# Kernel tuning notes

Hardware: AMD Instinct MI355X
Metric: run time of the kernel (lower is better)

The kernel has to match this reference:

```python
import jax, jax.numpy as jnp
import numpy as np

B_, S_, D_ = 2, 1024, 768
EXPAND, HEADDIM, DSTATE = 2, 64, 64
DINNER = EXPAND * D_            # 1536
NHEADS = DINNER // HEADDIM      # 24
DMLP = int(2.5 * D_)            # 1920
PROJ = 2 * DINNER + 2 * NHEADS * DSTATE + NHEADS + NHEADS * (DSTATE // 2)  # 6936


def rms_norm(x, w, eps=1e-5):
    return x * jax.lax.rsqrt(jnp.mean(x * x, axis=-1, keepdims=True) + eps) * w


def apply_rope(x, angles):
    # x: (..., d_state), angles: (..., d_state//2)
    x1 = x[..., 0::2]
    x2 = x[..., 1::2]
    c, s = jnp.cos(angles), jnp.sin(angles)
    even = c * x1 - s * x2
    odd = s * x1 + c * x2
    return jnp.stack([even, odd], axis=-1).reshape(x.shape)


def ssm_scan(x, A, Bm, Cm):
    # x: (b,s,h,p), A: (b,s,h), Bm/Cm: (b,s,h,n)
    b, s, h, p = x.shape
    n = Bm.shape[-1]

    def step(hstate, inp):
        x_t, A_t, B_t, C_t = inp
        hstate = hstate * jnp.exp(A_t)[:, :, None, None] + jnp.einsum('bhn,bhp->bhpn', B_t, x_t)
        y_t = jnp.einsum('bhpn,bhn->bhp', hstate, C_t)
        return hstate, y_t

    h0 = jnp.zeros((b, h, p, n), dtype=x.dtype)
    xs = (jnp.swapaxes(x, 0, 1), jnp.swapaxes(A, 0, 1),
          jnp.swapaxes(Bm, 0, 1), jnp.swapaxes(Cm, 0, 1))
    _, ys = jax.lax.scan(step, h0, xs)
    return jnp.swapaxes(ys, 0, 1)  # (b,s,h,p)


def setup_inputs() -> dict:
    key = jax.random.key(0)
    ks = jax.random.split(key, 16)
    sc = 0.02
    return {
        'x': jax.random.normal(ks[0], (B_, S_, D_), dtype=jnp.float32),
        'norm1_w': jnp.ones((D_,), jnp.float32),
        'norm2_w': jnp.ones((D_,), jnp.float32),
        'in_proj_w': jax.random.normal(ks[1], (PROJ, D_), jnp.float32) * sc,
        'out_proj_w': jax.random.normal(ks[2], (D_, DINNER), jnp.float32) * sc,
        'A_log': jax.random.uniform(ks[3], (NHEADS,), jnp.float32, -4.0, -1.0),
        'D': jnp.ones((NHEADS,), jnp.float32),
        'dt_bias': jax.random.uniform(ks[4], (NHEADS,), jnp.float32, 0.001, 0.1),
        'B_bias': jnp.ones((1, NHEADS, DSTATE), jnp.float32),
        'C_bias': jnp.ones((1, NHEADS, DSTATE), jnp.float32),
        'Bnorm_w': jnp.ones((DSTATE,), jnp.float32),
        'Cnorm_w': jnp.ones((DSTATE,), jnp.float32),
        'mlp_gate_w': jax.random.normal(ks[5], (DMLP, D_), jnp.float32) * sc,
        'mlp_up_w': jax.random.normal(ks[6], (DMLP, D_), jnp.float32) * sc,
        'mlp_down_w': jax.random.normal(ks[7], (D_, DMLP), jnp.float32) * sc,
    }


def reference(x, norm1_w, norm2_w, in_proj_w, out_proj_w, A_log, D, dt_bias,
              B_bias, C_bias, Bnorm_w, Cnorm_w, mlp_gate_w, mlp_up_w, mlp_down_w):
    b, s, _ = x.shape
    h = rms_norm(x, norm1_w)
    proj = jnp.einsum('bsd,od->bso', h, in_proj_w)
    i = 0
    z = proj[..., i:i + DINNER]; i += DINNER
    x_ssm = proj[..., i:i + DINNER]; i += DINNER
    Bm = proj[..., i:i + NHEADS * DSTATE].reshape(b, s, NHEADS, DSTATE); i += NHEADS * DSTATE
    Cm = proj[..., i:i + NHEADS * DSTATE].reshape(b, s, NHEADS, DSTATE); i += NHEADS * DSTATE
    dt = proj[..., i:i + NHEADS]; i += NHEADS
    theta = proj[..., i:].reshape(b, s, NHEADS, DSTATE // 2)

    dt = jax.nn.softplus(dt + dt_bias)                 # (b,s,h)
    A = -jnp.exp(A_log) * dt                           # (b,s,h)
    alpha = jnp.exp(A)
    gamma = (alpha - 1.0) / (A + 1e-6) * 0.5 + 1.0

    Bm = rms_norm(Bm, Bnorm_w) + B_bias
    Cm = rms_norm(Cm, Cnorm_w) + C_bias
    cum_theta = jnp.cumsum(dt[..., None] * theta, axis=1)
    Bm = apply_rope(Bm, cum_theta)
    Cm = apply_rope(Cm, cum_theta)

    x_ssm = x_ssm.reshape(b, s, NHEADS, HEADDIM)
    x_scaled = x_ssm * gamma[..., None]
    y = ssm_scan(x_scaled, A, Bm, Cm)                  # (b,s,h,p)
    skip = (D[None, None, :] * x_ssm.sum(-1))[..., None]  # (b,s,h,1)
    y = (y + skip).reshape(b, s, DINNER)
    y = y * (z * jax.nn.sigmoid(z))
    y = jnp.einsum('bsi,oi->bso', y, out_proj_w)
    x = x + y
    h2 = rms_norm(x, norm2_w)
    g = jnp.einsum('bsd,od->bso', h2, mlp_gate_w)
    u = jnp.einsum('bsd,od->bso', h2, mlp_up_w)
    mlp = jnp.einsum('bsi,oi->bso', (g * jax.nn.sigmoid(g)) * u, mlp_down_w)
    return x + mlp
```

## Files before the change

kernel.cpp:

```cpp
#include <hip/hip_runtime.h>

typedef unsigned short u16;
typedef __attribute__((ext_vector_type(8))) short short8;
typedef __attribute__((ext_vector_type(4))) float f32x4;

constexpr int B_N    = 2;
constexpr int SEQ    = 1024;
constexpr int DMODEL = 768;
constexpr int DINNER = 1536;
constexpr int NH     = 24;
constexpr int DMLP   = 1920;
constexpr int NPROJ  = 6936;
constexpr int PP     = 7040;
constexpr int MROWS  = B_N * SEQ;
constexpr int NCHUNK = 16;
constexpr int CLEN   = 64;

__device__ __forceinline__ u16 f2bf(float f) {
  union { float f; unsigned u; } x; x.f = f;
  unsigned r = x.u + 0x7fffu + ((x.u >> 16) & 1u);
  return (u16)(r >> 16);
}
__device__ __forceinline__ float bf2f(u16 b) {
  union { unsigned u; float f; } x; x.u = ((unsigned)b) << 16; return x.f;
}

__device__ __forceinline__ void gld_lds16(const u16* g, u16* l) {
  __builtin_amdgcn_global_load_lds((const __attribute__((address_space(1))) void*)g,
                                   (__attribute__((address_space(3))) void*)l, 16, 0, 0);
}

__device__ __forceinline__ short8 frag(const u16* base, int row, int cb) {
  return *(const short8*)(base + row * 64 + ((cb ^ (row & 7)) << 3));
}
__device__ __forceinline__ int swz_idx(int row, int e) {
  return (((e >> 3) ^ (row & 7)) << 3) | (e & 7);
}

constexpr size_t E0  = (size_t)PP * DMODEL;
constexpr size_t E0s = (size_t)NPROJ * DMODEL;
constexpr size_t E1  = (size_t)DMODEL * DINNER;
constexpr size_t E2  = (size_t)DMLP * DMODEL;
constexpr size_t ETOT = E0 + E1 + 3 * E2;

__global__ void cast_all_kernel(const float* __restrict__ w_in, const float* __restrict__ w_out,
                                const float* __restrict__ w_g, const float* __restrict__ w_u,
                                const float* __restrict__ w_d,
                                u16* __restrict__ wb_in, u16* __restrict__ wb_out,
                                u16* __restrict__ wb_gu, u16* __restrict__ wb_d) {
  size_t i = ((size_t)blockIdx.x * 256 + threadIdx.x) * 4;
  if (i >= ETOT) return;
  float4 v; u16* dst;
  if (i < E0) {
    dst = wb_in + i;
    if (i < E0s) v = *(const float4*)(w_in + i);
    else { v.x = v.y = v.z = v.w = 0.f; }
  } else if (i < E0 + E1) {
    size_t k = i - E0; dst = wb_out + k; v = *(const float4*)(w_out + k);
  } else if (i < E0 + E1 + 2 * E2) {
    size_t k = i - E0 - E1;
    size_t r = k / DMODEL, col = k - r * DMODEL;
    const float* src = (r & 1) ? w_u : w_g;
    v = *(const float4*)(src + (r >> 1) * DMODEL + col);
    dst = wb_gu + k;
  } else {
    size_t k = i - E0 - E1 - 2 * E2; dst = wb_d + k; v = *(const float4*)(w_d + k);
  }
  short4 o;
  o.x = (short)f2bf(v.x); o.y = (short)f2bf(v.y);
  o.z = (short)f2bf(v.z); o.w = (short)f2bf(v.w);
  *(short4*)dst = o;
}

__global__ __launch_bounds__(256) void add_rmsnorm_kernel(
    const float* __restrict__ a, const float* __restrict__ b,
    const float* __restrict__ w, float* __restrict__ sum_out,
    u16* __restrict__ hout) {
  int row = blockIdx.x;
  int t = threadIdx.x;
  const float* pa = a + (size_t)row * DMODEL;
  const float* pb = b ? b + (size_t)row * DMODEL : nullptr;
  float v[3]; float ss = 0.f;
#pragma unroll
  for (int i = 0; i < 3; ++i) {
    int c = t + i * 256;
    float x = pa[c];
    if (pb) x += pb[c];
    v[i] = x; ss += x * x;
  }
#pragma unroll
  for (int o = 32; o > 0; o >>= 1) ss += __shfl_xor(ss, o);
  __shared__ float red[4];
  if ((t & 63) == 0) red[t >> 6] = ss;
  __syncthreads();
  ss = red[0] + red[1] + red[2] + red[3];
  float sc = rsqrtf(ss * (1.f / DMODEL) + 1e-5f);
#pragma unroll
  for (int i = 0; i < 3; ++i) {
    int c = t + i * 256;
    if (sum_out) sum_out[(size_t)row * DMODEL + c] = v[i];
    hout[(size_t)row * DMODEL + c] = f2bf(v[i] * sc * w[c]);
  }
}

template<int BM, int MODE>
__global__ __launch_bounds__(256) void gemm_bt_kernel(
    const u16* __restrict__ A, const u16* __restrict__ Bw,
    void* __restrict__ Cv, int K, int ldc, const float* __restrict__ addsrc) {
  constexpr int MI = BM / 32;
  __shared__ u16 As[BM * 64];
  __shared__ u16 Bs[128 * 64];
  const int t = threadIdx.x;
  const int lane = t & 63;
  const int wave = t >> 6;
  const int wm = wave >> 1, wn = wave & 1;
  const int gx = gridDim.x, gy = gridDim.y;
  const int o = blockIdx.y * gx + blockIdx.x;
  const int nwg = gx * gy;
  const int cid = (o & 7) * (nwg >> 3) + (o >> 3);
  const int bx = cid / gy, by = cid - bx * gy;
  const int m0 = by * BM, n0 = bx * 128;
  f32x4 acc[MI][4] = {};
  const int rr = t >> 3;
  const int kc = (t & 7) * 8;
  const u16* ga = A + (size_t)(m0 + rr) * K + kc;
  const u16* gb = Bw + (size_t)(n0 + rr) * K + kc;
  for (int kt = 0; kt < K; kt += 64) {
    __syncthreads();
#pragma unroll
    for (int i = 0; i < MI; ++i)
      gld_lds16(ga + (size_t)i * 32 * K + kt, As + i * 2048 + t * 8);
#pragma unroll
    for (int i = 0; i < 4; ++i)
      gld_lds16(gb + (size_t)i * 32 * K + kt, Bs + i * 2048 + t * 8);
    __syncthreads();
#pragma unroll
    for (int kh = 0; kh < 2; ++kh) {
      short8 af[MI], bfr[4];
#pragma unroll
      for (int i = 0; i < MI; ++i)
        af[i] = *(const short8*)(As + (wm * (BM / 2) + i * 16 + (lane & 15)) * 64 + kh * 32 + (lane >> 4) * 8);
#pragma unroll
      for (int j = 0; j < 4; ++j)
        bfr[j] = *(const short8*)(Bs + (wn * 64 + j * 16 + (lane & 15)) * 64 + kh * 32 + (lane >> 4) * 8);
#pragma unroll
      for (int i = 0; i < MI; ++i)
#pragma unroll
        for (int j = 0; j < 4; ++j)
          acc[i][j] = __builtin_amdgcn_mfma_f32_16x16x32_bf16(af[i], bfr[j], acc[i][j], 0, 0, 0);
    }
  }
  const int cr = (lane >> 4) * 4;
  const int cc = lane & 15;
#pragma unroll
  for (int i = 0; i < MI; ++i) {
#pragma unroll
    for (int j = 0; j < 4; ++j) {
      int row = m0 + wm * (BM / 2) + i * 16 + cr;
      int col = n0 + wn * 64 + j * 16 + cc;
      if (MODE == 0) {
        float* C = (float*)Cv;
        float* cp = C + (size_t)row * ldc + col;
        if (addsrc) {
          const float* ap = addsrc + (size_t)row * ldc + col;
#pragma unroll
          for (int r = 0; r < 4; ++r) cp[(size_t)r * ldc] = acc[i][j][r] + ap[(size_t)r * ldc];
        } else {
#pragma unroll
          for (int r = 0; r < 4; ++r) cp[(size_t)r * ldc] = acc[i][j][r];
        }
      } else if (MODE == 1) {
        u16* C = (u16*)Cv;
#pragma unroll
        for (int r = 0; r < 4; ++r)
          C[(size_t)(row + r) * ldc + col] = f2bf(acc[i][j][r]);
      } else {
        u16* C = (u16*)Cv;
#pragma unroll
        for (int r = 0; r < 4; ++r) {
          float v = acc[i][j][r];
          float p = __shfl_xor(v, 1);
          if ((lane & 1) == 0) {
            float g = v, u = p;
            float res = g / (1.f + expf(-g)) * u;
            C[(size_t)(row + r) * ldc + (col >> 1)] = f2bf(res);
          }
        }
      }
    }
  }
}

__global__ __launch_bounds__(256) void prep_kernel(
    u16* __restrict__ proj, const float* __restrict__ A_log,
    const float* __restrict__ Dv, const float* __restrict__ dt_bias,
    const float* __restrict__ B_bias, const float* __restrict__ C_bias,
    const float* __restrict__ Bnw, const float* __restrict__ Cnw,
    float* __restrict__ Abuf, float* __restrict__ skip_b,
    float* __restrict__ dtheta) {
  int wid = blockIdx.x * 4 + (threadIdx.x >> 6);
  int lane = threadIdx.x & 63;
  int m = wid / NH, h = wid - m * NH;
  u16* row = proj + (size_t)m * PP;

  float Braw = bf2f(row[3072 + h * 64 + lane]);
  float Craw = bf2f(row[4608 + h * 64 + lane]);
  float sb = Braw * Braw, sc2 = Craw * Craw;
#pragma unroll
  for (int o = 32; o > 0; o >>= 1) { sb += __shfl_xor(sb, o); sc2 += __shfl_xor(sc2, o); }
  float rb = rsqrtf(sb * (1.f / 64.f) + 1e-5f);
  float rc = rsqrtf(sc2 * (1.f / 64.f) + 1e-5f);
  row[3072 + h * 64 + lane] = f2bf(Braw * rb * Bnw[lane] + B_bias[h * 64 + lane]);
  row[4608 + h * 64 + lane] = f2bf(Craw * rc * Cnw[lane] + C_bias[h * 64 + lane]);

  float dtr = bf2f(row[6144 + h]) + dt_bias[h];
  float dt = dtr > 20.f ? dtr : log1pf(expf(dtr));
  float A = -expf(A_log[h]) * dt;
  float alpha = expf(A);
  float gamma = (alpha - 1.f) / (A + 1e-6f) * 0.5f + 1.f;

  float xv = bf2f(row[1536 + h * 64 + lane]);
  float sx = xv;
#pragma unroll
  for (int o = 32; o > 0; o >>= 1) sx += __shfl_xor(sx, o);
  row[1536 + h * 64 + lane] = f2bf(xv * gamma);

  if (lane == 0) {
    Abuf[(size_t)m * NH + h] = A;
    skip_b[(size_t)m * NH + h] = Dv[h] * sx;
  }
  if (lane < 32) {
    float th = bf2f(row[6168 + h * 32 + lane]);
    dtheta[(size_t)m * 768 + h * 32 + lane] = dt * th;
  }
}

__global__ __launch_bounds__(256) void cumsum_a_kernel(float* __restrict__ dtheta,
                                                       float* __restrict__ ctot) {
  int bid = blockIdx.x;
  int cb = bid % 3, rest = bid / 3;
  int c = rest & 15, b = rest >> 4;
  int col = cb * 256 + threadIdx.x;
  float* p = dtheta + ((size_t)(b * SEQ + c * CLEN)) * 768 + col;
  float acc = 0.f;
#pragma unroll 4
  for (int s = 0; s < CLEN; ++s) {
    acc += p[(size_t)s * 768];
    p[(size_t)s * 768] = acc;
  }
  ctot[((size_t)b * NCHUNK + c) * 768 + col] = acc;
}

__global__ void cumsum_b_kernel(float* __restrict__ ctot) {
  int tid = blockIdx.x * 256 + threadIdx.x;
  int b = tid / 768, col = tid - b * 768;
  float pre = 0.f;
#pragma unroll
  for (int c = 0; c < NCHUNK; ++c) {
    size_t o = ((size_t)b * NCHUNK + c) * 768 + col;
    float v = ctot[o];
    ctot[o] = pre;
    pre += v;
  }
}

__global__ __launch_bounds__(256) void houtA_kernel(
    const u16* __restrict__ proj, const float* __restrict__ Abuf,
    const float* __restrict__ dtheta, const float* __restrict__ ctot,
    float* __restrict__ Lbuf, float* __restrict__ Hbuf) {
  int c = blockIdx.x & 15, bh = blockIdx.x >> 4;
  int b = bh / NH, h = bh - b * NH;
  int t = threadIdx.x, w = t >> 6, l = t & 63;
  __shared__ float sTmp[64][65];
  __shared__ u16 sBT[64 * 64];
  __shared__ u16 sXT[64 * 64];
  __shared__ float sRatio[64];
  int m0 = b * SEQ + c * CLEN;
  if (w == 0) {
    float v = Abuf[(size_t)(m0 + l) * NH + h];
#pragma unroll
    for (int o = 1; o < 64; o <<= 1) {
      float u = __shfl_up(v, o);
      if (l >= o) v += u;
    }
    Lbuf[(size_t)(m0 + l) * NH + h] = v;
    float L63 = __shfl(v, 63);
    sRatio[l] = expf(L63 - v);
  }
  int rr = t >> 2, q = t & 3;
  {
    const u16* row = proj + (size_t)(m0 + rr) * PP + 3072 + h * 64;
    const float* ang = dtheta + (size_t)(m0 + rr) * 768 + h * 32;
    const float* angc = ctot + ((size_t)(b * NCHUNK + c)) * 768 + h * 32;
#pragma unroll
    for (int k = 0; k < 4; ++k) {
      int e = q * 16 + k * 4;
      short4 sv = *(const short4*)(row + e);
      int j0 = e >> 1;
      float s0, c0, s1, c1;
      sincosf(ang[j0] + angc[j0], &s0, &c0);
      sincosf(ang[j0 + 1] + angc[j0 + 1], &s1, &c1);
      float vx = bf2f((u16)sv.x), vy = bf2f((u16)sv.y);
      float vz = bf2f((u16)sv.z), vw = bf2f((u16)sv.w);
      float4 ov;
      ov.x = c0 * vx - s0 * vy; ov.y = s0 * vx + c0 * vy;
      ov.z = c1 * vz - s1 * vw; ov.w = s1 * vz + c1 * vw;
      *(float4*)&sTmp[rr][e] = ov;
    }
  }
  __syncthreads();
  {
#pragma unroll
    for (int k = 0; k < 8; ++k) {
      int tw = (l + w * 8 + k) & 31;
      int t0 = tw * 2;
      unsigned pk = (unsigned)f2bf(sTmp[t0][l]) | ((unsigned)f2bf(sTmp[t0 + 1][l]) << 16);
      *(unsigned*)(sBT + l * 64 + swz_idx(l, t0)) = pk;
    }
  }
  __syncthreads();
  {
    const u16* row = proj + (size_t)(m0 + rr) * PP + 1536 + h * 64;
#pragma unroll
    for (int k = 0; k < 4; ++k) {
      int e = q * 16 + k * 4;
      short4 sv = *(const short4*)(row + e);
      float4 ov;
      ov.x = bf2f((u16)sv.x); ov.y = bf2f((u16)sv.y);
      ov.z = bf2f((u16)sv.z); ov.w = bf2f((u16)sv.w);
      *(float4*)&sTmp[rr][e] = ov;
    }
  }
  __syncthreads();
  {
#pragma unroll
    for (int k = 0; k < 8; ++k) {
      int tw = (l + w * 8 + k) & 31;
      int t0 = tw * 2;
      float v0 = sTmp[t0][l] * sRatio[t0];
      float v1 = sTmp[t0 + 1][l] * sRatio[t0 + 1];
      unsigned pk = (unsigned)f2bf(v0) | ((unsigned)f2bf(v1) << 16);
      *(unsigned*)(sXT + l * 64 + swz_idx(l, t0)) = pk;
    }
  }
  __syncthreads();
  f32x4 acc[4] = {};
#pragma unroll
  for (int kh = 0; kh < 2; ++kh) {
    int cb = kh * 4 + (l >> 4);
    short8 af = frag(sXT, w * 16 + (l & 15), cb);
#pragma unroll
    for (int j = 0; j < 4; ++j)
      acc[j] = __builtin_amdgcn_mfma_f32_16x16x32_bf16(af, frag(sBT, j * 16 + (l & 15), cb), acc[j], 0, 0, 0);
  }
  float* Hp = Hbuf + ((size_t)(bh * NCHUNK + c)) * 4096;
  int pr = w * 16 + ((l >> 4) << 2);
#pragma unroll
  for (int j = 0; j < 4; ++j)
#pragma unroll
    for (int r = 0; r < 4; ++r)
      Hp[(size_t)(pr + r) * 64 + j * 16 + (l & 15)] = acc[j][r];
}

__global__ __launch_bounds__(256) void scan2_kernel(
    float* __restrict__ Hbuf, const float* __restrict__ Lbuf) {
  int bh = blockIdx.x;
  int b = bh / NH, h = bh - b * NH;
  int e = threadIdx.x * 16;
  float S[16];
#pragma unroll
  for (int j = 0; j < 16; ++j) S[j] = 0.f;
  for (int c = 0; c < NCHUNK; ++c) {
    float* Hp = Hbuf + ((size_t)(bh * NCHUNK + c)) * 4096 + e;
    float P = expf(Lbuf[(size_t)(b * SEQ + c * CLEN + CLEN - 1) * NH + h]);
#pragma unroll
    for (int j = 0; j < 16; j += 4) {
      float4 loc = *(float4*)(Hp + j);
      float4 sv; sv.x = S[j]; sv.y = S[j + 1]; sv.z = S[j + 2]; sv.w = S[j + 3];
      *(float4*)(Hp + j) = sv;
      S[j]     = P * S[j]     + loc.x;
      S[j + 1] = P * S[j + 1] + loc.y;
      S[j + 2] = P * S[j + 2] + loc.z;
      S[j + 3] = P * S[j + 3] + loc.w;
    }
  }
}

__global__ __launch_bounds__(256) void intraB_kernel(
    const u16* __restrict__ proj, const float* __restrict__ Hbuf,
    const float* __restrict__ Lbuf, const float* __restrict__ skip_b,
    const float* __restrict__ dtheta, const float* __restrict__ ctot,
    u16* __restrict__ actb) {
  int c = blockIdx.x & 15, bh = blockIdx.x >> 4;
  int b = bh / NH, h = bh - b * NH;
  int t = threadIdx.x, w = t >> 6, l = t & 63;
  __shared__ u16 sC[64 * 64];
  __shared__ u16 sBH[64 * 64];
  __shared__ u16 sXT[64 * 64];
  __shared__ union UU { float tmp[64][65]; u16 gm[64 * 64]; } uS;
  __shared__ float sL[64], sSkip[64];
  int m0 = b * SEQ + c * CLEN;
  if (w == 0) {
    sL[l] = Lbuf[(size_t)(m0 + l) * NH + h];
    sSkip[l] = skip_b[(size_t)(m0 + l) * NH + h];
  }
  int rr = t >> 2, q = t & 3;
  const float* ang = dtheta + (size_t)(m0 + rr) * 768 + h * 32;
  const float* angc = ctot + ((size_t)(b * NCHUNK + c)) * 768 + h * 32;
  {
    const u16* rowC = proj + (size_t)(m0 + rr) * PP + 4608 + h * 64;
    const u16* rowX = proj + (size_t)(m0 + rr) * PP + 1536 + h * 64;
#pragma unroll
    for (int k = 0; k < 4; ++k) {
      int e = q * 16 + k * 4;
      short4 sv = *(const short4*)(rowC + e);
      int j0 = e >> 1;
      float s0, c0, s1, c1;
      sincosf(ang[j0] + angc[j0], &s0, &c0);
      sincosf(ang[j0 + 1] + angc[j0 + 1], &s1, &c1);
      float vx = bf2f((u16)sv.x), vy = bf2f((u16)sv.y);
      float vz = bf2f((u16)sv.z), vw = bf2f((u16)sv.w);
      unsigned lo = (unsigned)f2bf(c0 * vx - s0 * vy) | ((unsigned)f2bf(s0 * vx + c0 * vy) << 16);
      unsigned hi = (unsigned)f2bf(c1 * vz - s1 * vw) | ((unsigned)f2bf(s1 * vz + c1 * vw) << 16);
      int idx = swz_idx(rr, e);
      *(unsigned*)(sC + rr * 64 + idx) = lo;
      *(unsigned*)(sC + rr * 64 + idx + 2) = hi;
      short4 xv = *(const short4*)(rowX + e);
      float4 ov;
      ov.x = bf2f((u16)xv.x); ov.y = bf2f((u16)xv.y);
      ov.z = bf2f((u16)xv.z); ov.w = bf2f((u16)xv.w);
      *(float4*)&uS.tmp[rr][e] = ov;
    }
  }
  __syncthreads();
  {
#pragma unroll
    for (int k = 0; k < 8; ++k) {
      int tw = (l + w * 8 + k) & 31;
      int t0 = tw * 2;
      unsigned pk = (unsigned)f2bf(uS.tmp[t0][l]) | ((unsigned)f2bf(uS.tmp[t0 + 1][l]) << 16);
      *(unsigned*)(sXT + l * 64 + swz_idx(l, t0)) = pk;
    }
    const u16* rowB = proj + (size_t)(m0 + rr) * PP + 3072 + h * 64;
#pragma unroll
    for (int k = 0; k < 4; ++k) {
      int e = q * 16 + k * 4;
      short4 sv = *(const short4*)(rowB + e);
      int j0 = e >> 1;
      float s0, c0, s1, c1;
      sincosf(ang[j0] + angc[j0], &s0, &c0);
      sincosf(ang[j0 + 1] + angc[j0 + 1], &s1, &c1);
      float vx = bf2f((u16)sv.x), vy = bf2f((u16)sv.y);
      float vz = bf2f((u16)sv.z), vw = bf2f((u16)sv.w);
      unsigned lo = (unsigned)f2bf(c0 * vx - s0 * vy) | ((unsigned)f2bf(s0 * vx + c0 * vy) << 16);
      unsigned hi = (unsigned)f2bf(c1 * vz - s1 * vw) | ((unsigned)f2bf(s1 * vz + c1 * vw) << 16);
      int idx = swz_idx(rr, e);
      *(unsigned*)(sBH + rr * 64 + idx) = lo;
      *(unsigned*)(sBH + rr * 64 + idx + 2) = hi;
    }
  }
  __syncthreads();
  f32x4 g4[4] = {};
#pragma unroll
  for (int kh = 0; kh < 2; ++kh) {
    int cb = kh * 4 + (l >> 4);
    short8 af = frag(sC, w * 16 + (l & 15), cb);
#pragma unroll
    for (int j = 0; j < 4; ++j)
      g4[j] = __builtin_amdgcn_mfma_f32_16x16x32_bf16(af, frag(sBH, j * 16 + (l & 15), cb), g4[j], 0, 0, 0);
  }
  __syncthreads();
  {
    int sr = w * 16 + ((l >> 4) << 2);
#pragma unroll
    for (int j = 0; j < 4; ++j) {
      int tc = j * 16 + (l & 15);
#pragma unroll
      for (int r = 0; r < 4; ++r) {
        int s = sr + r;
        float gv = (tc <= s) ? g4[j][r] * expf(sL[s] - sL[tc]) : 0.f;
        uS.gm[s * 64 + swz_idx(s, tc)] = f2bf(gv);
      }
    }
    const float* Hp = Hbuf + ((size_t)(bh * NCHUNK + c)) * 4096 + rr * 64;
#pragma unroll
    for (int k = 0; k < 4; ++k) {
      int e = q * 16 + k * 4;
      float4 v = *(const float4*)(Hp + e);
      unsigned lo = (unsigned)f2bf(v.x) | ((unsigned)f2bf(v.y) << 16);
      unsigned hi = (unsigned)f2bf(v.z) | ((unsigned)f2bf(v.w) << 16);
      int idx = swz_idx(rr, e);
      *(unsigned*)(sBH + rr * 64 + idx) = lo;
      *(unsigned*)(sBH + rr * 64 + idx + 2) = hi;
    }
  }
  __syncthreads();
  f32x4 y1[4] = {}, y2[4] = {};
#pragma unroll
  for (int kh = 0; kh < 2; ++kh) {
    int cb = kh * 4 + (l >> 4);
    short8 ag = frag(uS.gm, w * 16 + (l & 15), cb);
    short8 ac = frag(sC, w * 16 + (l & 15), cb);
#pragma unroll
    for (int j = 0; j < 4; ++j) {
      y1[j] = __builtin_amdgcn_mfma_f32_16x16x32_bf16(ag, frag(sXT, j * 16 + (l & 15), cb), y1[j], 0, 0, 0);
      y2[j] = __builtin_amdgcn_mfma_f32_16x16x32_bf16(ac, frag(sBH, j * 16 + (l & 15), cb), y2[j], 0, 0, 0);
    }
  }
  int sr = w * 16 + ((l >> 4) << 2);
#pragma unroll
  for (int r = 0; r < 4; ++r) {
    int s = sr + r;
    float scale = expf(sL[s]);
    float skp = sSkip[s];
    size_t mrow = (size_t)(m0 + s);
#pragma unroll
    for (int j = 0; j < 4; ++j) {
      int p = j * 16 + (l & 15);
      float y = y1[j][r] + scale * y2[j][r] + skp;
      float z = bf2f(proj[mrow * PP + h * 64 + p]);
      float sg = 1.f / (1.f + expf(-z));
      actb[mrow * DINNER + h * 64 + p] = f2bf(y * z * sg);
    }
  }
}

extern "C" void kernel_launch(void* const* d_in, const int* in_sizes, int n_in,
                              void* d_out, int out_size, void* d_ws, size_t ws_size,
                              hipStream_t stream) {
  (void)in_sizes; (void)n_in; (void)out_size; (void)ws_size;
  const float* x      = (const float*)d_in[0];
  const float* n1w    = (const float*)d_in[1];
  const float* n2w    = (const float*)d_in[2];
  const float* w_in   = (const float*)d_in[3];
  const float* w_out  = (const float*)d_in[4];
  const float* A_log  = (const float*)d_in[5];
  const float* Dv     = (const float*)d_in[6];
  const float* dt_b   = (const float*)d_in[7];
  const float* B_bias = (const float*)d_in[8];
  const float* C_bias = (const float*)d_in[9];
  const float* Bnw    = (const float*)d_in[10];
  const float* Cnw    = (const float*)d_in[11];
  const float* w_g    = (const float*)d_in[12];
  const float* w_u    = (const float*)d_in[13];
  const float* w_d    = (const float*)d_in[14];
  float* out = (float*)d_out;

  char* ws = (char*)d_ws;
  size_t off = 0;
  auto alloc = [&](size_t bytes) -> char* {
    char* p = ws + off;
    off = (off + bytes + 255) & ~(size_t)255;
    return p;
  };
  u16*   wb_in  = (u16*)  alloc(E0 * 2);
  u16*   wb_out = (u16*)  alloc(E1 * 2);
  u16*   wb_gu  = (u16*)  alloc(E2 * 2 * 2);
  u16*   wb_d   = (u16*)  alloc(E2 * 2);
  u16*   h1     = (u16*)  alloc((size_t)MROWS * DMODEL * 2);
  u16*   proj   = (u16*)  alloc((size_t)MROWS * PP * 2);
  float* Abuf   = (float*)alloc((size_t)MROWS * NH * 4);
  float* skip_b = (float*)alloc((size_t)MROWS * NH * 4);
  float* Lbuf   = (float*)alloc((size_t)MROWS * NH * 4);
  float* dtheta = (float*)alloc((size_t)MROWS * 768 * 4);
  float* ctot   = (float*)alloc((size_t)B_N * NCHUNK * 768 * 4);
  float* Hbuf   = (float*)alloc((size_t)B_N * NH * NCHUNK * 4096 * 4);
  u16*   actb   = (u16*)  alloc((size_t)MROWS * DINNER * 2);
  float* tmp1   = (float*)alloc((size_t)MROWS * DMODEL * 4);
  float* x2     = (float*)alloc((size_t)MROWS * DMODEL * 4);
  u16*   h2     = (u16*)  alloc((size_t)MROWS * DMODEL * 2);
  u16*   gub    = (u16*)  alloc((size_t)MROWS * DMLP * 2);

  cast_all_kernel<<<(int)((ETOT / 4 + 255) / 256), 256, 0, stream>>>(
      w_in, w_out, w_g, w_u, w_d, wb_in, wb_out, wb_gu, wb_d);
  add_rmsnorm_kernel<<<MROWS, 256, 0, stream>>>(x, nullptr, n1w, nullptr, h1);
  {
    dim3 g(PP / 128, MROWS / 128);
    gemm_bt_kernel<128, 1><<<g, 256, 0, stream>>>(h1, wb_in, proj, DMODEL, PP, nullptr);
  }
  prep_kernel<<<MROWS * NH / 4, 256, 0, stream>>>(proj, A_log, Dv, dt_b, B_bias, C_bias,
                                                  Bnw, Cnw, Abuf, skip_b, dtheta);
  cumsum_a_kernel<<<B_N * NCHUNK * 3, 256, 0, stream>>>(dtheta, ctot);
  cumsum_b_kernel<<<6, 256, 0, stream>>>(ctot);
  houtA_kernel<<<B_N * NH * NCHUNK, 256, 0, stream>>>(proj, Abuf, dtheta, ctot, Lbuf, Hbuf);
  scan2_kernel<<<B_N * NH, 256, 0, stream>>>(Hbuf, Lbuf);
  intraB_kernel<<<B_N * NH * NCHUNK, 256, 0, stream>>>(proj, Hbuf, Lbuf, skip_b,
                                                       dtheta, ctot, actb);
  {
    dim3 g(DMODEL / 128, MROWS / 64);
    gemm_bt_kernel<64, 0><<<g, 256, 0, stream>>>(actb, wb_out, tmp1, DINNER, DMODEL, nullptr);
  }
  add_rmsnorm_kernel<<<MROWS, 256, 0, stream>>>(x, tmp1, n2w, x2, h2);
  {
    dim3 g(2 * DMLP / 128, MROWS / 128);
    gemm_bt_kernel<128, 2><<<g, 256, 0, stream>>>(h2, wb_gu, gub, DMODEL, DMLP, nullptr);
  }
  {
    dim3 g(DMODEL / 128, MROWS / 64);
    gemm_bt_kernel<64, 0><<<g, 256, 0, stream>>>(gub, wb_d, out, DMLP, DMODEL, x2);
  }
}
```

Before: 333.5 us.

## Add standalone RoPE kernel, shrink GEMM tiles, widen scan2 grid, use fast exp

Several changes at once. RoPE on B and C now runs once in a dedicated kernel that writes back into proj, instead of being recomputed with sincosf in both houtA and intraB. The GEMMs gain a BN template parameter and use smaller 64x128 or 64x64 tiles, giving more workgroups on the many-CU GPU. scan2 now uses one thread per state element across 16x more blocks. expf calls are swapped for __expf and __sincosf, trading some accuracy for cheaper transcendentals, and the extra kernel adds one more pass over proj.

```diff
diff --git a/kernel.cpp b/kernel.cpp
--- a/kernel.cpp
+++ b/kernel.cpp
@@ -103,13 +103,14 @@
   }
 }
 
-template<int BM, int MODE>
+template<int BM, int BN, int MODE>
 __global__ __launch_bounds__(256) void gemm_bt_kernel(
     const u16* __restrict__ A, const u16* __restrict__ Bw,
     void* __restrict__ Cv, int K, int ldc, const float* __restrict__ addsrc) {
   constexpr int MI = BM / 32;
+  constexpr int NJ = BN / 32;
   __shared__ u16 As[BM * 64];
-  __shared__ u16 Bs[128 * 64];
+  __shared__ u16 Bs[BN * 64];
   const int t = threadIdx.x;
   const int lane = t & 63;
   const int wave = t >> 6;
@@ -119,8 +120,8 @@
   const int nwg = gx * gy;
   const int cid = (o & 7) * (nwg >> 3) + (o >> 3);
   const int bx = cid / gy, by = cid - bx * gy;
-  const int m0 = by * BM, n0 = bx * 128;
-  f32x4 acc[MI][4] = {};
+  const int m0 = by * BM, n0 = bx * BN;
+  f32x4 acc[MI][NJ] = {};
   const int rr = t >> 3;
   const int kc = (t & 7) * 8;
   const u16* ga = A + (size_t)(m0 + rr) * K + kc;
@@ -131,22 +132,22 @@
     for (int i = 0; i < MI; ++i)
       gld_lds16(ga + (size_t)i * 32 * K + kt, As + i * 2048 + t * 8);
 #pragma unroll
-    for (int i = 0; i < 4; ++i)
+    for (int i = 0; i < NJ; ++i)
       gld_lds16(gb + (size_t)i * 32 * K + kt, Bs + i * 2048 + t * 8);
     __syncthreads();
 #pragma unroll
     for (int kh = 0; kh < 2; ++kh) {
-      short8 af[MI], bfr[4];
+      short8 af[MI], bfr[NJ];
 #pragma unroll
       for (int i = 0; i < MI; ++i)
         af[i] = *(const short8*)(As + (wm * (BM / 2) + i * 16 + (lane & 15)) * 64 + kh * 32 + (lane >> 4) * 8);
 #pragma unroll
-      for (int j = 0; j < 4; ++j)
-        bfr[j] = *(const short8*)(Bs + (wn * 64 + j * 16 + (lane & 15)) * 64 + kh * 32 + (lane >> 4) * 8);
+      for (int j = 0; j < NJ; ++j)
+        bfr[j] = *(const short8*)(Bs + (wn * (BN / 2) + j * 16 + (lane & 15)) * 64 + kh * 32 + (lane >> 4) * 8);
 #pragma unroll
       for (int i = 0; i < MI; ++i)
 #pragma unroll
-        for (int j = 0; j < 4; ++j)
+        for (int j = 0; j < NJ; ++j)
           acc[i][j] = __builtin_amdgcn_mfma_f32_16x16x32_bf16(af[i], bfr[j], acc[i][j], 0, 0, 0);
     }
   }
@@ -155,9 +156,9 @@
 #pragma unroll
   for (int i = 0; i < MI; ++i) {
 #pragma unroll
-    for (int j = 0; j < 4; ++j) {
+    for (int j = 0; j < NJ; ++j) {
       int row = m0 + wm * (BM / 2) + i * 16 + cr;
-      int col = n0 + wn * 64 + j * 16 + cc;
+      int col = n0 + wn * (BN / 2) + j * 16 + cc;
       if (MODE == 0) {
         float* C = (float*)Cv;
         float* cp = C + (size_t)row * ldc + col;
@@ -182,7 +183,7 @@
           float p = __shfl_xor(v, 1);
           if ((lane & 1) == 0) {
             float g = v, u = p;
-            float res = g / (1.f + expf(-g)) * u;
+            float res = g / (1.f + __expf(-g)) * u;
             C[(size_t)(row + r) * ldc + (col >> 1)] = f2bf(res);
           }
         }
@@ -214,9 +215,9 @@
   row[4608 + h * 64 + lane] = f2bf(Craw * rc * Cnw[lane] + C_bias[h * 64 + lane]);
 
   float dtr = bf2f(row[6144 + h]) + dt_bias[h];
-  float dt = dtr > 20.f ? dtr : log1pf(expf(dtr));
-  float A = -expf(A_log[h]) * dt;
-  float alpha = expf(A);
+  float dt = dtr > 20.f ? dtr : log1pf(__expf(dtr));
+  float A = -__expf(A_log[h]) * dt;
+  float alpha = __expf(A);
   float gamma = (alpha - 1.f) / (A + 1e-6f) * 0.5f + 1.f;
 
   float xv = bf2f(row[1536 + h * 64 + lane]);
@@ -264,9 +265,29 @@
   }
 }
 
+__global__ __launch_bounds__(256) void rope_kernel(
+    u16* __restrict__ proj, const float* __restrict__ dtheta,
+    const float* __restrict__ ctot) {
+  int wid = blockIdx.x * 4 + (threadIdx.x >> 6);
+  int lane = threadIdx.x & 63;
+  int m = wid / NH, h = wid - m * NH;
+  int j = lane & 31;
+  int b = m >> 10;
+  int c = (m >> 6) & 15;
+  float ang = dtheta[(size_t)m * 768 + h * 32 + j] +
+              ctot[((size_t)b * NCHUNK + c) * 768 + h * 32 + j];
+  float sn, cs;
+  __sincosf(ang, &sn, &cs);
+  int base = (lane < 32) ? 3072 : 4608;
+  unsigned* p = (unsigned*)(proj + (size_t)m * PP + base + h * 64) + j;
+  unsigned v = *p;
+  float x1 = bf2f((u16)(v & 0xffffu));
+  float x2 = bf2f((u16)(v >> 16));
+  *p = (unsigned)f2bf(cs * x1 - sn * x2) | ((unsigned)f2bf(sn * x1 + cs * x2) << 16);
+}
+
 __global__ __launch_bounds__(256) void houtA_kernel(
     const u16* __restrict__ proj, const float* __restrict__ Abuf,
-    const float* __restrict__ dtheta, const float* __restrict__ ctot,
     float* __restrict__ Lbuf, float* __restrict__ Hbuf) {
   int c = blockIdx.x & 15, bh = blockIdx.x >> 4;
   int b = bh / NH, h = bh - b * NH;
@@ -285,42 +306,11 @@
     }
     Lbuf[(size_t)(m0 + l) * NH + h] = v;
     float L63 = __shfl(v, 63);
-    sRatio[l] = expf(L63 - v);
+    sRatio[l] = __expf(L63 - v);
   }
   int rr = t >> 2, q = t & 3;
   {
     const u16* row = proj + (size_t)(m0 + rr) * PP + 3072 + h * 64;
-    const float* ang = dtheta + (size_t)(m0 + rr) * 768 + h * 32;
-    const float* angc = ctot + ((size_t)(b * NCHUNK + c)) * 768 + h * 32;
-#pragma unroll
-    for (int k = 0; k < 4; ++k) {
-      int e = q * 16 + k * 4;
-      short4 sv = *(const short4*)(row + e);
-      int j0 = e >> 1;
-      float s0, c0, s1, c1;
-      sincosf(ang[j0] + angc[j0], &s0, &c0);
-      sincosf(ang[j0 + 1] + angc[j0 + 1], &s1, &c1);
-      float vx = bf2f((u16)sv.x), vy = bf2f((u16)sv.y);
-      float vz = bf2f((u16)sv.z), vw = bf2f((u16)sv.w);
-      float4 ov;
-      ov.x = c0 * vx - s0 * vy; ov.y = s0 * vx + c0 * vy;
-      ov.z = c1 * vz - s1 * vw; ov.w = s1 * vz + c1 * vw;
-      *(float4*)&sTmp[rr][e] = ov;
-    }
-  }
-  __syncthreads();
-  {
-#pragma unroll
-    for (int k = 0; k < 8; ++k) {
-      int tw = (l + w * 8 + k) & 31;
-      int t0 = tw * 2;
-      unsigned pk = (unsigned)f2bf(sTmp[t0][l]) | ((unsigned)f2bf(sTmp[t0 + 1][l]) << 16);
-      *(unsigned*)(sBT + l * 64 + swz_idx(l, t0)) = pk;
-    }
-  }
-  __syncthreads();
-  {
-    const u16* row = proj + (size_t)(m0 + rr) * PP + 1536 + h * 64;
 #pragma unroll
     for (int k = 0; k < 4; ++k) {
       int e = q * 16 + k * 4;
@@ -337,6 +327,29 @@
     for (int k = 0; k < 8; ++k) {
       int tw = (l + w * 8 + k) & 31;
       int t0 = tw * 2;
+      unsigned pk = (unsigned)f2bf(sTmp[t0][l]) | ((unsigned)f2bf(sTmp[t0 + 1][l]) << 16);
+      *(unsigned*)(sBT + l * 64 + swz_idx(l, t0)) = pk;
+    }
+  }
+  __syncthreads();
+  {
+    const u16* row = proj + (size_t)(m0 + rr) * PP + 1536 + h * 64;
+#pragma unroll
+    for (int k = 0; k < 4; ++k) {
+      int e = q * 16 + k * 4;
+      short4 sv = *(const short4*)(row + e);
+      float4 ov;
+      ov.x = bf2f((u16)sv.x); ov.y = bf2f((u16)sv.y);
+      ov.z = bf2f((u16)sv.z); ov.w = bf2f((u16)sv.w);
+      *(float4*)&sTmp[rr][e] = ov;
+    }
+  }
+  __syncthreads();
+  {
+#pragma unroll
+    for (int k = 0; k < 8; ++k) {
+      int tw = (l + w * 8 + k) & 31;
+      int t0 = tw * 2;
       float v0 = sTmp[t0][l] * sRatio[t0];
       float v1 = sTmp[t0 + 1][l] * sRatio[t0 + 1];
       unsigned pk = (unsigned)f2bf(v0) | ((unsigned)f2bf(v1) << 16);
@@ -364,32 +377,22 @@
 
 __global__ __launch_bounds__(256) void scan2_kernel(
     float* __restrict__ Hbuf, const float* __restrict__ Lbuf) {
-  int bh = blockIdx.x;
+  int bh = blockIdx.x >> 4;
+  int e = (blockIdx.x & 15) * 256 + threadIdx.x;
   int b = bh / NH, h = bh - b * NH;
-  int e = threadIdx.x * 16;
-  float S[16];
-#pragma unroll
-  for (int j = 0; j < 16; ++j) S[j] = 0.f;
+  float S = 0.f;
   for (int c = 0; c < NCHUNK; ++c) {
     float* Hp = Hbuf + ((size_t)(bh * NCHUNK + c)) * 4096 + e;
-    float P = expf(Lbuf[(size_t)(b * SEQ + c * CLEN + CLEN - 1) * NH + h]);
-#pragma unroll
-    for (int j = 0; j < 16; j += 4) {
-      float4 loc = *(float4*)(Hp + j);
-      float4 sv; sv.x = S[j]; sv.y = S[j + 1]; sv.z = S[j + 2]; sv.w = S[j + 3];
-      *(float4*)(Hp + j) = sv;
-      S[j]     = P * S[j]     + loc.x;
-      S[j + 1] = P * S[j + 1] + loc.y;
-      S[j + 2] = P * S[j + 2] + loc.z;
-      S[j + 3] = P * S[j + 3] + loc.w;
-    }
+    float P = __expf(Lbuf[(size_t)(b * SEQ + c * CLEN + CLEN - 1) * NH + h]);
+    float v = *Hp;
+    *Hp = S;
+    S = P * S + v;
   }
 }
 
 __global__ __launch_bounds__(256) void intraB_kernel(
     const u16* __restrict__ proj, const float* __restrict__ Hbuf,
     const float* __restrict__ Lbuf, const float* __restrict__ skip_b,
-    const float* __restrict__ dtheta, const float* __restrict__ ctot,
     u16* __restrict__ actb) {
   int c = blockIdx.x & 15, bh = blockIdx.x >> 4;
   int b = bh / NH, h = bh - b * NH;
@@ -405,26 +408,20 @@
     sSkip[l] = skip_b[(size_t)(m0 + l) * NH + h];
   }
   int rr = t >> 2, q = t & 3;
-  const float* ang = dtheta + (size_t)(m0 + rr) * 768 + h * 32;
-  const float* angc = ctot + ((size_t)(b * NCHUNK + c)) * 768 + h * 32;
   {
     const u16* rowC = proj + (size_t)(m0 + rr) * PP + 4608 + h * 64;
+    const u16* rowB = proj + (size_t)(m0 + rr) * PP + 3072 + h * 64;
     const u16* rowX = proj + (size_t)(m0 + rr) * PP + 1536 + h * 64;
 #pragma unroll
     for (int k = 0; k < 4; ++k) {
       int e = q * 16 + k * 4;
-      short4 sv = *(const short4*)(rowC + e);
-      int j0 = e >> 1;
-      float s0, c0, s1, c1;
-      sincosf(ang[j0] + angc[j0], &s0, &c0);
-      sincosf(ang[j0 + 1] + angc[j0 + 1], &s1, &c1);
-      float vx = bf2f((u16)sv.x), vy = bf2f((u16)sv.y);
-      float vz = bf2f((u16)sv.z), vw = bf2f((u16)sv.w);
-      unsigned lo = (unsigned)f2bf(c0 * vx - s0 * vy) | ((unsigned)f2bf(s0 * vx + c0 * vy) << 16);
-      unsigned hi = (unsigned)f2bf(c1 * vz - s1 * vw) | ((unsigned)f2bf(s1 * vz + c1 * vw) << 16);
       int idx = swz_idx(rr, e);
-      *(unsigned*)(sC + rr * 64 + idx) = lo;
-      *(unsigned*)(sC + rr * 64 + idx + 2) = hi;
+      short4 cv = *(const short4*)(rowC + e);
+      *(unsigned*)(sC + rr * 64 + idx)     = (unsigned)(u16)cv.x | ((unsigned)(u16)cv.y << 16);
+      *(unsigned*)(sC + rr * 64 + idx + 2) = (unsigned)(u16)cv.z | ((unsigned)(u16)cv.w << 16);
+      short4 bv = *(const short4*)(rowB + e);
+      *(unsigned*)(sBH + rr * 64 + idx)     = (unsigned)(u16)bv.x | ((unsigned)(u16)bv.y << 16);
+      *(unsigned*)(sBH + rr * 64 + idx + 2) = (unsigned)(u16)bv.z | ((unsigned)(u16)bv.w << 16);
       short4 xv = *(const short4*)(rowX + e);
       float4 ov;
       ov.x = bf2f((u16)xv.x); ov.y = bf2f((u16)xv.y);
@@ -441,23 +438,6 @@
       unsigned pk = (unsigned)f2bf(uS.tmp[t0][l]) | ((unsigned)f2bf(uS.tmp[t0 + 1][l]) << 16);
       *(unsigned*)(sXT + l * 64 + swz_idx(l, t0)) = pk;
     }
-    const u16* rowB = proj + (size_t)(m0 + rr) * PP + 3072 + h * 64;
-#pragma unroll
-    for (int k = 0; k < 4; ++k) {
-      int e = q * 16 + k * 4;
-      short4 sv = *(const short4*)(rowB + e);
-      int j0 = e >> 1;
-      float s0, c0, s1, c1;
-      sincosf(ang[j0] + angc[j0], &s0, &c0);
-      sincosf(ang[j0 + 1] + angc[j0 + 1], &s1, &c1);
-      float vx = bf2f((u16)sv.x), vy = bf2f((u16)sv.y);
-      float vz = bf2f((u16)sv.z), vw = bf2f((u16)sv.w);
-      unsigned lo = (unsigned)f2bf(c0 * vx - s0 * vy) | ((unsigned)f2bf(s0 * vx + c0 * vy) << 16);
-      unsigned hi = (unsigned)f2bf(c1 * vz - s1 * vw) | ((unsigned)f2bf(s1 * vz + c1 * vw) << 16);
-      int idx = swz_idx(rr, e);
-      *(unsigned*)(sBH + rr * 64 + idx) = lo;
-      *(unsigned*)(sBH + rr * 64 + idx + 2) = hi;
-    }
   }
   __syncthreads();
   f32x4 g4[4] = {};
@@ -478,7 +458,7 @@
 #pragma unroll
       for (int r = 0; r < 4; ++r) {
         int s = sr + r;
-        float gv = (tc <= s) ? g4[j][r] * expf(sL[s] - sL[tc]) : 0.f;
+        float gv = (tc <= s) ? g4[j][r] * __expf(sL[s] - sL[tc]) : 0.f;
         uS.gm[s * 64 + swz_idx(s, tc)] = f2bf(gv);
       }
     }
@@ -511,7 +491,7 @@
 #pragma unroll
   for (int r = 0; r < 4; ++r) {
     int s = sr + r;
-    float scale = expf(sL[s]);
+    float scale = __expf(sL[s]);
     float skp = sSkip[s];
     size_t mrow = (size_t)(m0 + s);
 #pragma unroll
@@ -519,7 +499,7 @@
       int p = j * 16 + (l & 15);
       float y = y1[j][r] + scale * y2[j][r] + skp;
       float z = bf2f(proj[mrow * PP + h * 64 + p]);
-      float sg = 1.f / (1.f + expf(-z));
+      float sg = 1.f / (1.f + __expf(-z));
       actb[mrow * DINNER + h * 64 + p] = f2bf(y * z * sg);
     }
   }
@@ -575,28 +555,28 @@
       w_in, w_out, w_g, w_u, w_d, wb_in, wb_out, wb_gu, wb_d);
   add_rmsnorm_kernel<<<MROWS, 256, 0, stream>>>(x, nullptr, n1w, nullptr, h1);
   {
-    dim3 g(PP / 128, MROWS / 128);
-    gemm_bt_kernel<128, 1><<<g, 256, 0, stream>>>(h1, wb_in, proj, DMODEL, PP, nullptr);
+    dim3 g(PP / 128, MROWS / 64);
+    gemm_bt_kernel<64, 128, 1><<<g, 256, 0, stream>>>(h1, wb_in, proj, DMODEL, PP, nullptr);
   }
   prep_kernel<<<MROWS * NH / 4, 256, 0, stream>>>(proj, A_log, Dv, dt_b, B_bias, C_bias,
                                                   Bnw, Cnw, Abuf, skip_b, dtheta);
   cumsum_a_kernel<<<B_N * NCHUNK * 3, 256, 0, stream>>>(dtheta, ctot);
   cumsum_b_kernel<<<6, 256, 0, stream>>>(ctot);
-  houtA_kernel<<<B_N * NH * NCHUNK, 256, 0, stream>>>(proj, Abuf, dtheta, ctot, Lbuf, Hbuf);
-  scan2_kernel<<<B_N * NH, 256, 0, stream>>>(Hbuf, Lbuf);
-  intraB_kernel<<<B_N * NH * NCHUNK, 256, 0, stream>>>(proj, Hbuf, Lbuf, skip_b,
-                                                       dtheta, ctot, actb);
-  {
-    dim3 g(DMODEL / 128, MROWS / 64);
-    gemm_bt_kernel<64, 0><<<g, 256, 0, stream>>>(actb, wb_out, tmp1, DINNER, DMODEL, nullptr);
+  rope_kernel<<<MROWS * NH / 4, 256, 0, stream>>>(proj, dtheta, ctot);
+  houtA_kernel<<<B_N * NH * NCHUNK, 256, 0, stream>>>(proj, Abuf, Lbuf, Hbuf);
+  scan2_kernel<<<B_N * NH * NCHUNK, 256, 0, stream>>>(Hbuf, Lbuf);
+  intraB_kernel<<<B_N * NH * NCHUNK, 256, 0, stream>>>(proj, Hbuf, Lbuf, skip_b, actb);
+  {
+    dim3 g(DMODEL / 64, MROWS / 64);
+    gemm_bt_kernel<64, 64, 0><<<g, 256, 0, stream>>>(actb, wb_out, tmp1, DINNER, DMODEL, nullptr);
   }
   add_rmsnorm_kernel<<<MROWS, 256, 0, stream>>>(x, tmp1, n2w, x2, h2);
   {
-    dim3 g(2 * DMLP / 128, MROWS / 128);
-    gemm_bt_kernel<128, 2><<<g, 256, 0, stream>>>(h2, wb_gu, gub, DMODEL, DMLP, nullptr);
-  }
-  {
-    dim3 g(DMODEL / 128, MROWS / 64);
-    gemm_bt_kernel<64, 0><<<g, 256, 0, stream>>>(gub, wb_d, out, DMLP, DMODEL, x2);
-  }
-}
+    dim3 g(2 * DMLP / 128, MROWS / 64);
+    gemm_bt_kernel<64, 128, 2><<<g, 256, 0, stream>>>(h2, wb_gu, gub, DMODEL, DMLP, nullptr);
+  }
+  {
+    dim3 g(DMODEL / 64, MROWS / 64);
+    gemm_bt_kernel<64, 64, 0><<<g, 256, 0, stream>>>(gub, wb_d, out, DMLP, DMODEL, x2);
+  }
+}
```

New measurement: 295.3 us. -11.5%, faster.
